# Kernel optimization log

Hardware: AMD Instinct MI355X
Metric: run time of the kernel (lower is better)

Reference implementation:

```python
import jax, jax.numpy as jnp
import numpy as np

D_MODEL, N_HEADS = 1024, 16
HEAD_DIM = D_MODEL // N_HEADS  # 64
BS, Q_LEN, SEQ_LEN = 4, 1024, 1024


def setup_inputs() -> dict:
    key = jax.random.key(0)
    kq, kk, kv, kp, km = jax.random.split(key, 5)
    q = jax.random.normal(kq, (BS, N_HEADS, Q_LEN, HEAD_DIM), dtype=jnp.float32)
    k = jax.random.normal(kk, (BS, N_HEADS, HEAD_DIM, SEQ_LEN), dtype=jnp.float32)
    v = jax.random.normal(kv, (BS, N_HEADS, SEQ_LEN, HEAD_DIM), dtype=jnp.float32)
    prev = jax.random.normal(kp, (BS, N_HEADS, Q_LEN, SEQ_LEN), dtype=jnp.float32)
    attn_weighted_mask = jax.random.uniform(km, (1, N_HEADS, Q_LEN, SEQ_LEN), dtype=jnp.float32)
    scale = jnp.asarray(HEAD_DIM ** (-0.5), dtype=jnp.float32)  # nn.Parameter scalar
    return {"q": q, "k": k, "v": v, "prev": prev,
            "attn_weighted_mask": attn_weighted_mask, "scale": scale}


def reference(q, k, v, prev, attn_weighted_mask, scale):
    # scores = (q @ k) * scale + prev       [bs, h, q_len, seq_len]
    attn_scores = jnp.einsum('bhqd,bhds->bhqs', q, k) * scale + prev
    # softmax over keys; attn_dropout p=0.0 -> identity
    attn_weights = jax.nn.softmax(attn_scores, axis=-1)
    # post-softmax elementwise weighted mask
    attn_weights = attn_weights * attn_weighted_mask
    # output = attn_weights @ v             [bs, h, q_len, d_v]
    output = jnp.einsum('bhqs,bhsd->bhqd', attn_weights, v)
    # res_attention=True -> also return weights and pre-softmax scores
    return output, attn_weights, attn_scores
```

## Files before the change

### kernel.cpp

```cpp
#include <hip/hip_runtime.h>


#define QL 1024
#define SL 1024
#define HD 64

typedef __attribute__((ext_vector_type(8))) short bf16x8;
typedef __attribute__((ext_vector_type(4))) short bf16x4;
typedef __attribute__((ext_vector_type(4))) float f32x4;

__device__ __forceinline__ short f2bf(float f) {
    union { float f; unsigned u; } v; v.f = f;
    unsigned r = v.u + 0x7FFFu + ((v.u >> 16) & 1u);
    return (short)(r >> 16);
}

__global__ __launch_bounds__(256) void _prepack_kv(
    const float* __restrict__ k, const float* __restrict__ v,
    short* __restrict__ ws)
{
    __shared__ short tile[64][72];
    const int t = threadIdx.x;
    int b = blockIdx.x;
    const float* src; short* dst; int ld_src, ld_dst;
    if (b < 1024) {
        const int bh = b >> 4, st = b & 15;
        src = k + (size_t)bh * 65536 + st * 64;               ld_src = 1024;
        dst = ws + (size_t)bh * 65536 + (size_t)st * 4096;    ld_dst = 64;
    } else {
        b -= 1024;
        const int bh = b >> 4, st = b & 15;
        src = v + (size_t)bh * 65536 + (size_t)st * 4096;     ld_src = 64;
        dst = ws + 4194304 + (size_t)bh * 65536 + st * 64;    ld_dst = 1024;
    }
    {
        const int r = t >> 2, c0 = (t & 3) * 16;
#pragma unroll
        for (int i = 0; i < 4; ++i) {
            float4 f = *(const float4*)&src[(size_t)r * ld_src + c0 + 4 * i];
            bf16x4 s4 = { f2bf(f.x), f2bf(f.y), f2bf(f.z), f2bf(f.w) };
            *(bf16x4*)&tile[r][c0 + 4 * i] = s4;
        }
    }
    __syncthreads();
    {
        const int r = t >> 2, c0 = (t & 3) * 16;
        bf16x8 o0, o1;
#pragma unroll
        for (int j = 0; j < 8; ++j) o0[j] = tile[c0 + j][r];
#pragma unroll
        for (int j = 0; j < 8; ++j) o1[j] = tile[c0 + 8 + j][r];
        *(bf16x8*)&dst[(size_t)r * ld_dst + c0]     = o0;
        *(bf16x8*)&dst[(size_t)r * ld_dst + c0 + 8] = o1;
    }
}

__global__ __launch_bounds__(512, 6) void _attn_main(
    const float* __restrict__ q, const float* __restrict__ prev,
    const float* __restrict__ mask, const float* __restrict__ scale_p,
    const short* __restrict__ Kt, const short* __restrict__ Vt,
    float* __restrict__ out)
{
    __shared__ short wbuf[16384];
    __shared__ float red[128];
    __shared__ float obuf[1024];

    const int tid  = threadIdx.x;
    const int w    = tid >> 6;
    const int lane = tid & 63;
    const int quad = lane >> 4;
    const int lp   = lane & 15;

    const int blk = (blockIdx.x & 7) * 512 + (blockIdx.x >> 3);
    const int bh  = blk >> 6;
    const int qt  = blk & 63;
    const int h   = bh & 15;
    const int q0  = qt * 16;

    const float scale = scale_p[0];

    const float* Qb = q    + (size_t)bh * QL * HD + (size_t)q0 * HD;
    const float* Pb = prev + (size_t)bh * QL * SL + (size_t)q0 * SL;
    const float* Mb = mask + (size_t)h  * QL * SL + (size_t)q0 * SL;
    const short* Kb = Kt + (size_t)bh * (SL * HD);
    const short* Vb = Vt + (size_t)bh * (SL * HD);

    float* Ob   = out            + (size_t)bh * QL * HD + (size_t)q0 * HD;
    float* Wout = out + 4194304  + (size_t)bh * QL * SL + (size_t)q0 * SL;
    float* Sout = out + 71303168 + (size_t)bh * QL * SL + (size_t)q0 * SL;

    const int s0 = 128 * w;
    const int sq = s0 + quad * 4;

    f32x4 acc[8];
    {
        const float* pp = Pb + (size_t)lp * SL + sq;
#pragma unroll
        for (int t = 0; t < 8; ++t)
            acc[t] = *(const f32x4*)(pp + 16 * t);
    }

    bf16x8 aq[2];
#pragma unroll
    for (int ks = 0; ks < 2; ++ks) {
        const float* qp = Qb + (size_t)lp * HD + ks * 32 + quad * 8;
        float4 a = *(const float4*)qp;
        float4 b = *(const float4*)(qp + 4);
        aq[ks][0] = f2bf(a.x * scale); aq[ks][1] = f2bf(a.y * scale);
        aq[ks][2] = f2bf(a.z * scale); aq[ks][3] = f2bf(a.w * scale);
        aq[ks][4] = f2bf(b.x * scale); aq[ks][5] = f2bf(b.y * scale);
        aq[ks][6] = f2bf(b.z * scale); aq[ks][7] = f2bf(b.w * scale);
    }

#pragma unroll
    for (int ks = 0; ks < 2; ++ks) {
#pragma unroll
        for (int t = 0; t < 8; ++t) {
            bf16x8 bk = *(const bf16x8*)&Kb[(size_t)(s0 + 16 * t + lp) * HD
                                            + ks * 32 + quad * 8];
            acc[t] = __builtin_amdgcn_mfma_f32_16x16x32_bf16(bk, aq[ks], acc[t], 0, 0, 0);
        }
    }

    float4 mkA[4];
    {
        const float* mp = Mb + (size_t)lp * SL + sq;
#pragma unroll
        for (int t = 0; t < 4; ++t)
            mkA[t] = *(const float4*)(mp + 16 * t);
    }

    float lsum = 0.f;
    {
        float* sp = Sout + (size_t)lp * SL + sq;
#pragma unroll
        for (int t = 0; t < 8; ++t) {
            f32x4 sv = acc[t];
            *(f32x4*)(sp + 16 * t) = sv;
#pragma unroll
            for (int r = 0; r < 4; ++r) {
                float e = __expf(sv[r]);
                acc[t][r] = e;
                lsum += e;
            }
        }
    }
    lsum += __shfl_xor(lsum, 16);
    lsum += __shfl_xor(lsum, 32);
    if (lane < 16) red[w * 16 + lane] = lsum;
    __syncthreads();
    float rsum = 0.f;
#pragma unroll
    for (int u = 0; u < 8; ++u) rsum += red[u * 16 + lp];
    const float rinv = 1.0f / rsum;

    float4 mkB[4];
    {
        const float* mp = Mb + (size_t)lp * SL + sq + 64;
#pragma unroll
        for (int t = 0; t < 4; ++t)
            mkB[t] = *(const float4*)(mp + 16 * t);
    }

    {
        float* wp = Wout + (size_t)lp * SL + sq;
#pragma unroll
        for (int t = 0; t < 8; ++t) {
            float4 m4 = (t < 4) ? mkA[t] : mkB[t - 4];
            f32x4 wv;
#pragma unroll
            for (int r = 0; r < 4; ++r) wv[r] = acc[t][r] * rinv * m4[r];
            *(f32x4*)(wp + 16 * t) = wv;
            const int sb = sq + 16 * t;
            bf16x4 wb = { f2bf(wv[0]), f2bf(wv[1]), f2bf(wv[2]), f2bf(wv[3]) };
            *(bf16x4*)&wbuf[((sb >> 3) * 16 + lp) * 8 + (sb & 4)] = wb;
        }
    }
    __syncthreads();

    const int dgrp = w & 3;
    const int kh   = w >> 2;
    f32x4 oacc = {0.f, 0.f, 0.f, 0.f};
#pragma unroll 8
    for (int kk = 0; kk < 16; ++kk) {
        const int ks = kh * 16 + kk;
        bf16x8 aw = *(const bf16x8*)&wbuf[((ks * 4 + quad) * 16 + lp) * 8];
        bf16x8 bv = *(const bf16x8*)&Vb[(size_t)(16 * dgrp + lp) * SL
                                        + ks * 32 + quad * 8];
        oacc = __builtin_amdgcn_mfma_f32_16x16x32_bf16(bv, aw, oacc, 0, 0, 0);
    }
    if (kh == 1) {
        *(f32x4*)&obuf[lp * 64 + 16 * dgrp + quad * 4] = oacc;
    }
    __syncthreads();
    if (kh == 0) {
        f32x4 ov = *(const f32x4*)&obuf[lp * 64 + 16 * dgrp + quad * 4];
#pragma unroll
        for (int r = 0; r < 4; ++r) ov[r] += oacc[r];
        *(f32x4*)&Ob[(size_t)lp * HD + 16 * dgrp + quad * 4] = ov;
    }
}

__global__ __launch_bounds__(256) void _attn_fallback(
    const float* __restrict__ q, const float* __restrict__ k,
    const float* __restrict__ v, const float* __restrict__ prev,
    const float* __restrict__ mask, const float* __restrict__ scale_p,
    float* __restrict__ out)
{
    const int WSTR = SL + 8;
    __shared__ short wbuf[16 * (SL + 8)];
    __shared__ float red[4 * 16];

    const int tid  = threadIdx.x;
    const int w    = tid >> 6;
    const int lane = tid & 63;
    const int quad = lane >> 4;
    const int lp   = lane & 15;

    const int blk = blockIdx.x;
    const int bh  = blk >> 6;
    const int qt  = blk & 63;
    const int h   = bh & 15;
    const int q0  = qt * 16;

    const float scale = scale_p[0];

    const float* Qb = q    + (size_t)bh * QL * HD + (size_t)q0 * HD;
    const float* Kb = k    + (size_t)bh * HD * SL;
    const float* Vb = v    + (size_t)bh * SL * HD;
    const float* Pb = prev + (size_t)bh * QL * SL + (size_t)q0 * SL;
    const float* Mb = mask + (size_t)h  * QL * SL + (size_t)q0 * SL;

    float* Ob   = out            + (size_t)bh * QL * HD + (size_t)q0 * HD;
    float* Wout = out + 4194304  + (size_t)bh * QL * SL + (size_t)q0 * SL;
    float* Sout = out + 71303168 + (size_t)bh * QL * SL + (size_t)q0 * SL;

    bf16x8 aq[2];
#pragma unroll
    for (int ks = 0; ks < 2; ++ks) {
        const float* qp = Qb + (size_t)lp * HD + ks * 32 + quad * 8;
#pragma unroll
        for (int j = 0; j < 8; ++j) aq[ks][j] = f2bf(qp[j] * scale);
    }

    const int s0 = 256 * w;
    f32x4 acc[16];
#pragma unroll
    for (int t = 0; t < 16; ++t) {
#pragma unroll
        for (int r = 0; r < 4; ++r)
            acc[t][r] = Pb[(size_t)(quad * 4 + r) * SL + s0 + 16 * t + lp];
    }
#pragma unroll
    for (int ks = 0; ks < 2; ++ks) {
#pragma unroll
        for (int t = 0; t < 16; ++t) {
            bf16x8 bk;
            const float* kp = Kb + (size_t)(ks * 32 + quad * 8) * SL + s0 + 16 * t + lp;
#pragma unroll
            for (int j = 0; j < 8; ++j) bk[j] = f2bf(kp[(size_t)j * SL]);
            acc[t] = __builtin_amdgcn_mfma_f32_16x16x32_bf16(aq[ks], bk, acc[t], 0, 0, 0);
        }
    }

    float lsum[4] = {0.f, 0.f, 0.f, 0.f};
#pragma unroll
    for (int t = 0; t < 16; ++t) {
#pragma unroll
        for (int r = 0; r < 4; ++r) {
            float sv = acc[t][r];
            Sout[(size_t)(quad * 4 + r) * SL + s0 + 16 * t + lp] = sv;
            float e = __expf(sv);
            acc[t][r] = e;
            lsum[r] += e;
        }
    }
#pragma unroll
    for (int r = 0; r < 4; ++r) {
        float s = lsum[r];
        s += __shfl_xor(s, 1);  s += __shfl_xor(s, 2);
        s += __shfl_xor(s, 4);  s += __shfl_xor(s, 8);
        lsum[r] = s;
    }
    if (lp == 0) {
#pragma unroll
        for (int r = 0; r < 4; ++r) red[w * 16 + quad * 4 + r] = lsum[r];
    }
    __syncthreads();
    float rinv[4];
#pragma unroll
    for (int r = 0; r < 4; ++r) {
        float s = red[0 * 16 + quad * 4 + r] + red[1 * 16 + quad * 4 + r]
                + red[2 * 16 + quad * 4 + r] + red[3 * 16 + quad * 4 + r];
        rinv[r] = 1.0f / s;
    }

#pragma unroll
    for (int t = 0; t < 16; ++t) {
#pragma unroll
        for (int r = 0; r < 4; ++r) {
            int row = quad * 4 + r;
            int col = s0 + 16 * t + lp;
            float wv = acc[t][r] * rinv[r] * Mb[(size_t)row * SL + col];
            Wout[(size_t)row * SL + col] = wv;
            wbuf[row * WSTR + col] = f2bf(wv);
        }
    }
    __syncthreads();

    f32x4 oacc = {0.f, 0.f, 0.f, 0.f};
#pragma unroll 4
    for (int ks = 0; ks < 32; ++ks) {
        bf16x8 aw = *(const bf16x8*)&wbuf[lp * WSTR + ks * 32 + quad * 8];
        bf16x8 bv;
        const float* vp = Vb + (size_t)(ks * 32 + quad * 8) * HD + 16 * w + lp;
#pragma unroll
        for (int j = 0; j < 8; ++j) bv[j] = f2bf(vp[(size_t)j * HD]);
        oacc = __builtin_amdgcn_mfma_f32_16x16x32_bf16(aw, bv, oacc, 0, 0, 0);
    }
#pragma unroll
    for (int r = 0; r < 4; ++r)
        Ob[(size_t)(quad * 4 + r) * HD + 16 * w + lp] = oacc[r];
}

extern "C" void kernel_launch(void* const* d_in, const int* in_sizes, int n_in,
                              void* d_out, int out_size, void* d_ws, size_t ws_size,
                              hipStream_t stream) {
    const float* q     = (const float*)d_in[0];
    const float* k     = (const float*)d_in[1];
    const float* v     = (const float*)d_in[2];
    const float* prev  = (const float*)d_in[3];
    const float* mask  = (const float*)d_in[4];
    const float* scale = (const float*)d_in[5];
    float* out = (float*)d_out;

    if (d_ws != nullptr && ws_size >= (size_t)16 * 1024 * 1024) {
        short* ws = (short*)d_ws;
        _prepack_kv<<<dim3(2048), dim3(256), 0, stream>>>(k, v, ws);
        _attn_main<<<dim3(4096), dim3(512), 0, stream>>>(
            q, prev, mask, scale, ws, ws + 4194304, out);
    } else {
        _attn_fallback<<<dim3(4096), dim3(256), 0, stream>>>(
            q, k, v, prev, mask, scale, out);
    }
}
```

Before: 927.0 us.

## Make attention blocks persistent over 8 query tiles with software-prefetched prev/Q

```diff
diff --git a/kernel.cpp b/kernel.cpp
--- a/kernel.cpp
+++ b/kernel.cpp
@@ -55,7 +55,7 @@
     }
 }
 
-__global__ __launch_bounds__(512, 6) void _attn_main(
+__global__ __launch_bounds__(512, 4) void _attn_main(
     const float* __restrict__ q, const float* __restrict__ prev,
     const float* __restrict__ mask, const float* __restrict__ scale_p,
     const short* __restrict__ Kt, const short* __restrict__ Vt,
@@ -71,133 +71,154 @@
     const int quad = lane >> 4;
     const int lp   = lane & 15;
 
-    const int blk = (blockIdx.x & 7) * 512 + (blockIdx.x >> 3);
-    const int bh  = blk >> 6;
-    const int qt  = blk & 63;
+    const int j   = blockIdx.x;
+    const int xcd = j & 7;
+    const int i6  = j >> 3;
+    const int bh  = xcd * 8 + (i6 >> 3);
+    const int sub = i6 & 7;
     const int h   = bh & 15;
-    const int q0  = qt * 16;
 
     const float scale = scale_p[0];
 
-    const float* Qb = q    + (size_t)bh * QL * HD + (size_t)q0 * HD;
-    const float* Pb = prev + (size_t)bh * QL * SL + (size_t)q0 * SL;
-    const float* Mb = mask + (size_t)h  * QL * SL + (size_t)q0 * SL;
-    const short* Kb = Kt + (size_t)bh * (SL * HD);
-    const short* Vb = Vt + (size_t)bh * (SL * HD);
-
-    float* Ob   = out            + (size_t)bh * QL * HD + (size_t)q0 * HD;
-    float* Wout = out + 4194304  + (size_t)bh * QL * SL + (size_t)q0 * SL;
-    float* Sout = out + 71303168 + (size_t)bh * QL * SL + (size_t)q0 * SL;
-
-    const int s0 = 128 * w;
-    const int sq = s0 + quad * 4;
-
-    f32x4 acc[8];
+    const float* Qbh = q    + (size_t)bh * QL * HD;
+    const float* Pbh = prev + (size_t)bh * QL * SL;
+    const float* Mbh = mask + (size_t)h  * QL * SL;
+    const short* Kb  = Kt + (size_t)bh * (SL * HD);
+    const short* Vb  = Vt + (size_t)bh * (SL * HD);
+
+    float* Obh = out            + (size_t)bh * QL * HD;
+    float* Wbh = out + 4194304  + (size_t)bh * QL * SL;
+    float* Sbh = out + 71303168 + (size_t)bh * QL * SL;
+
+    const int s0   = 128 * w;
+    const int sq   = s0 + quad * 4;
+    const int dgrp = w & 3;
+    const int kh   = w >> 2;
+
+    f32x4 accA[8], accB[8];
+    float4 qrA[4], qrB[4];
+
     {
-        const float* pp = Pb + (size_t)lp * SL + sq;
-#pragma unroll
-        for (int t = 0; t < 8; ++t)
-            acc[t] = *(const f32x4*)(pp + 16 * t);
-    }
-
-    bf16x8 aq[2];
-#pragma unroll
-    for (int ks = 0; ks < 2; ++ks) {
-        const float* qp = Qb + (size_t)lp * HD + ks * 32 + quad * 8;
-        float4 a = *(const float4*)qp;
-        float4 b = *(const float4*)(qp + 4);
-        aq[ks][0] = f2bf(a.x * scale); aq[ks][1] = f2bf(a.y * scale);
-        aq[ks][2] = f2bf(a.z * scale); aq[ks][3] = f2bf(a.w * scale);
-        aq[ks][4] = f2bf(b.x * scale); aq[ks][5] = f2bf(b.y * scale);
-        aq[ks][6] = f2bf(b.z * scale); aq[ks][7] = f2bf(b.w * scale);
-    }
-
-#pragma unroll
-    for (int ks = 0; ks < 2; ++ks) {
+        const int q0 = (sub * 8) * 16;
+        const float* pp = Pbh + (size_t)(q0 + lp) * SL + sq;
+#pragma unroll
+        for (int t = 0; t < 8; ++t) accA[t] = *(const f32x4*)(pp + 16 * t);
+        const float* qp = Qbh + (size_t)(q0 + lp) * HD + quad * 8;
+        qrA[0] = *(const float4*)qp;        qrA[1] = *(const float4*)(qp + 4);
+        qrA[2] = *(const float4*)(qp + 32); qrA[3] = *(const float4*)(qp + 36);
+    }
+
+    auto body = [&](f32x4 (&acc)[8], f32x4 (&accN)[8],
+                    float4 (&qr)[4], float4 (&qrN)[4], int i) {
+        const int q0  = (sub * 8 + i) * 16;
+        const int iN  = (i < 7) ? i + 1 : i;
+        const int q0N = (sub * 8 + iN) * 16;
+
+        bf16x8 aq0, aq1;
+        aq0[0] = f2bf(qr[0].x * scale); aq0[1] = f2bf(qr[0].y * scale);
+        aq0[2] = f2bf(qr[0].z * scale); aq0[3] = f2bf(qr[0].w * scale);
+        aq0[4] = f2bf(qr[1].x * scale); aq0[5] = f2bf(qr[1].y * scale);
+        aq0[6] = f2bf(qr[1].z * scale); aq0[7] = f2bf(qr[1].w * scale);
+        aq1[0] = f2bf(qr[2].x * scale); aq1[1] = f2bf(qr[2].y * scale);
+        aq1[2] = f2bf(qr[2].z * scale); aq1[3] = f2bf(qr[2].w * scale);
+        aq1[4] = f2bf(qr[3].x * scale); aq1[5] = f2bf(qr[3].y * scale);
+        aq1[6] = f2bf(qr[3].z * scale); aq1[7] = f2bf(qr[3].w * scale);
+
 #pragma unroll
         for (int t = 0; t < 8; ++t) {
-            bf16x8 bk = *(const bf16x8*)&Kb[(size_t)(s0 + 16 * t + lp) * HD
-                                            + ks * 32 + quad * 8];
-            acc[t] = __builtin_amdgcn_mfma_f32_16x16x32_bf16(bk, aq[ks], acc[t], 0, 0, 0);
-        }
-    }
-
-    float4 mkA[4];
-    {
-        const float* mp = Mb + (size_t)lp * SL + sq;
-#pragma unroll
-        for (int t = 0; t < 4; ++t)
-            mkA[t] = *(const float4*)(mp + 16 * t);
-    }
-
-    float lsum = 0.f;
-    {
-        float* sp = Sout + (size_t)lp * SL + sq;
+            bf16x8 bk = *(const bf16x8*)&Kb[(size_t)(s0 + 16 * t + lp) * HD + quad * 8];
+            acc[t] = __builtin_amdgcn_mfma_f32_16x16x32_bf16(bk, aq0, acc[t], 0, 0, 0);
+        }
 #pragma unroll
         for (int t = 0; t < 8; ++t) {
-            f32x4 sv = acc[t];
-            *(f32x4*)(sp + 16 * t) = sv;
+            bf16x8 bk = *(const bf16x8*)&Kb[(size_t)(s0 + 16 * t + lp) * HD + 32 + quad * 8];
+            acc[t] = __builtin_amdgcn_mfma_f32_16x16x32_bf16(bk, aq1, acc[t], 0, 0, 0);
+        }
+
+        {
+            float* sp = Sbh + (size_t)(q0 + lp) * SL + sq;
+#pragma unroll
+            for (int t = 0; t < 8; ++t) *(f32x4*)(sp + 16 * t) = acc[t];
+        }
+
+        {
+            const float* pp = Pbh + (size_t)(q0N + lp) * SL + sq;
+#pragma unroll
+            for (int t = 0; t < 8; ++t) accN[t] = *(const f32x4*)(pp + 16 * t);
+            const float* qp = Qbh + (size_t)(q0N + lp) * HD + quad * 8;
+            qrN[0] = *(const float4*)qp;        qrN[1] = *(const float4*)(qp + 4);
+            qrN[2] = *(const float4*)(qp + 32); qrN[3] = *(const float4*)(qp + 36);
+        }
+
+        float lsum = 0.f;
+#pragma unroll
+        for (int t = 0; t < 8; ++t) {
 #pragma unroll
             for (int r = 0; r < 4; ++r) {
-                float e = __expf(sv[r]);
+                float e = __expf(acc[t][r]);
                 acc[t][r] = e;
                 lsum += e;
             }
         }
-    }
-    lsum += __shfl_xor(lsum, 16);
-    lsum += __shfl_xor(lsum, 32);
-    if (lane < 16) red[w * 16 + lane] = lsum;
-    __syncthreads();
-    float rsum = 0.f;
-#pragma unroll
-    for (int u = 0; u < 8; ++u) rsum += red[u * 16 + lp];
-    const float rinv = 1.0f / rsum;
-
-    float4 mkB[4];
-    {
-        const float* mp = Mb + (size_t)lp * SL + sq + 64;
-#pragma unroll
-        for (int t = 0; t < 4; ++t)
-            mkB[t] = *(const float4*)(mp + 16 * t);
-    }
-
-    {
-        float* wp = Wout + (size_t)lp * SL + sq;
-#pragma unroll
-        for (int t = 0; t < 8; ++t) {
-            float4 m4 = (t < 4) ? mkA[t] : mkB[t - 4];
-            f32x4 wv;
-#pragma unroll
-            for (int r = 0; r < 4; ++r) wv[r] = acc[t][r] * rinv * m4[r];
-            *(f32x4*)(wp + 16 * t) = wv;
-            const int sb = sq + 16 * t;
-            bf16x4 wb = { f2bf(wv[0]), f2bf(wv[1]), f2bf(wv[2]), f2bf(wv[3]) };
-            *(bf16x4*)&wbuf[((sb >> 3) * 16 + lp) * 8 + (sb & 4)] = wb;
-        }
-    }
-    __syncthreads();
-
-    const int dgrp = w & 3;
-    const int kh   = w >> 2;
-    f32x4 oacc = {0.f, 0.f, 0.f, 0.f};
+
+        const float* mp = Mbh + (size_t)(q0 + lp) * SL + sq;
+        float4 mkA[4];
+#pragma unroll
+        for (int t = 0; t < 4; ++t) mkA[t] = *(const float4*)(mp + 16 * t);
+
+        lsum += __shfl_xor(lsum, 16);
+        lsum += __shfl_xor(lsum, 32);
+        if (lane < 16) red[w * 16 + lane] = lsum;
+        __syncthreads();
+        float rsum = 0.f;
+#pragma unroll
+        for (int u = 0; u < 8; ++u) rsum += red[u * 16 + lp];
+        const float rinv = 1.0f / rsum;
+
+        float4 mkB[4];
+#pragma unroll
+        for (int t = 0; t < 4; ++t) mkB[t] = *(const float4*)(mp + 64 + 16 * t);
+
+        {
+            float* wp = Wbh + (size_t)(q0 + lp) * SL + sq;
+#pragma unroll
+            for (int t = 0; t < 8; ++t) {
+                float4 m4 = (t < 4) ? mkA[t] : mkB[t - 4];
+                f32x4 wv;
+#pragma unroll
+                for (int r = 0; r < 4; ++r) wv[r] = acc[t][r] * rinv * m4[r];
+                *(f32x4*)(wp + 16 * t) = wv;
+                const int sb = sq + 16 * t;
+                bf16x4 wb = { f2bf(wv[0]), f2bf(wv[1]), f2bf(wv[2]), f2bf(wv[3]) };
+                *(bf16x4*)&wbuf[((sb >> 3) * 16 + lp) * 8 + (sb & 4)] = wb;
+            }
+        }
+        __syncthreads();
+
+        f32x4 oacc = {0.f, 0.f, 0.f, 0.f};
 #pragma unroll 8
-    for (int kk = 0; kk < 16; ++kk) {
-        const int ks = kh * 16 + kk;
-        bf16x8 aw = *(const bf16x8*)&wbuf[((ks * 4 + quad) * 16 + lp) * 8];
-        bf16x8 bv = *(const bf16x8*)&Vb[(size_t)(16 * dgrp + lp) * SL
-                                        + ks * 32 + quad * 8];
-        oacc = __builtin_amdgcn_mfma_f32_16x16x32_bf16(bv, aw, oacc, 0, 0, 0);
-    }
-    if (kh == 1) {
-        *(f32x4*)&obuf[lp * 64 + 16 * dgrp + quad * 4] = oacc;
-    }
-    __syncthreads();
-    if (kh == 0) {
-        f32x4 ov = *(const f32x4*)&obuf[lp * 64 + 16 * dgrp + quad * 4];
-#pragma unroll
-        for (int r = 0; r < 4; ++r) ov[r] += oacc[r];
-        *(f32x4*)&Ob[(size_t)lp * HD + 16 * dgrp + quad * 4] = ov;
+        for (int kk = 0; kk < 16; ++kk) {
+            const int ks = kh * 16 + kk;
+            bf16x8 aw = *(const bf16x8*)&wbuf[((ks * 4 + quad) * 16 + lp) * 8];
+            bf16x8 bv = *(const bf16x8*)&Vb[(size_t)(16 * dgrp + lp) * SL
+                                            + ks * 32 + quad * 8];
+            oacc = __builtin_amdgcn_mfma_f32_16x16x32_bf16(bv, aw, oacc, 0, 0, 0);
+        }
+        if (kh == 1) {
+            *(f32x4*)&obuf[lp * 64 + 16 * dgrp + quad * 4] = oacc;
+        }
+        __syncthreads();
+        if (kh == 0) {
+            f32x4 ov = *(const f32x4*)&obuf[lp * 64 + 16 * dgrp + quad * 4];
+#pragma unroll
+            for (int r = 0; r < 4; ++r) ov[r] += oacc[r];
+            *(f32x4*)&Obh[(size_t)(q0 + lp) * HD + 16 * dgrp + quad * 4] = ov;
+        }
+    };
+
+    for (int ii = 0; ii < 8; ii += 2) {
+        body(accA, accB, qrA, qrB, ii);
+        body(accB, accA, qrB, qrA, ii + 1);
     }
 }
 
@@ -337,7 +358,7 @@
     if (d_ws != nullptr && ws_size >= (size_t)16 * 1024 * 1024) {
         short* ws = (short*)d_ws;
         _prepack_kv<<<dim3(2048), dim3(256), 0, stream>>>(k, v, ws);
-        _attn_main<<<dim3(4096), dim3(512), 0, stream>>>(
+        _attn_main<<<dim3(512), dim3(512), 0, stream>>>(
             q, prev, mask, scale, ws, ws + 4194304, out);
     } else {
         _attn_fallback<<<dim3(4096), dim3(256), 0, stream>>>(
```

Measured after the change: 978.6 us. +5.6%, slower.
